# Kernel tuning notes

Hardware: AMD Instinct MI355X
Metric: run time of the kernel (lower is better)

Reference implementation:

```python
import jax, jax.numpy as jnp
import numpy as np

B = 32768
IN_DIM, OUT_DIM, VAR_DIM = 2, 3, 50
KER_DIMS = [1024, 1024, 1024, 1024]
NSTEPS = 32  # fixed-step RK4 stand-in for adaptive odeint over t in [0, 1]


def setup_inputs() -> dict:
    key = jax.random.key(0)
    ks = jax.random.split(key, 11)
    x = jax.random.normal(ks[0], (B, IN_DIM), dtype=jnp.float32)
    dims = [VAR_DIM] + KER_DIMS + [VAR_DIM]
    inp = {"x": x}
    for i, (d1, d2) in enumerate(zip(dims[:-1], dims[1:])):
        # torch Linear(d1+1, d2): weight (d2, d1+1); stored here as (d1+1, d2)
        bound = 1.0 / np.sqrt(d1 + 1)
        inp[f"W{i}"] = jax.random.uniform(ks[1 + 2 * i], (d1 + 1, d2), jnp.float32, -bound, bound)
        inp[f"b{i}"] = jax.random.uniform(ks[2 + 2 * i], (d2,), jnp.float32, -bound, bound)
    return inp


def _odefunc(t, y, Ws, bs):
    # Each layer: concat time column, Linear, ReLU (except last) -- matches ODEfunc.forward
    out = y
    n = len(Ws)
    for i in range(n):
        tcol = jnp.full((out.shape[0], 1), t, dtype=out.dtype)
        h = jnp.concatenate([out, tcol], axis=1)
        out = h @ Ws[i] + bs[i]
        if i < n - 1:
            out = jax.nn.relu(out)
    return out


def _integrate(x, Ws, bs):
    # Pad input into var_dim state: out[:, :in_dim] = x, rest zeros
    y0 = jnp.zeros((x.shape[0], VAR_DIM), dtype=x.dtype).at[:, : x.shape[1]].set(x)
    dt = jnp.asarray(1.0 / NSTEPS, dtype=x.dtype)
    ts = jnp.arange(NSTEPS, dtype=x.dtype) * dt

    def step(y, t):
        k1 = _odefunc(t, y, Ws, bs)
        k2 = _odefunc(t + dt * 0.5, y + dt * 0.5 * k1, Ws, bs)
        k3 = _odefunc(t + dt * 0.5, y + dt * 0.5 * k2, Ws, bs)
        k4 = _odefunc(t + dt, y + dt * k3, Ws, bs)
        return y + (dt / 6.0) * (k1 + 2.0 * k2 + 2.0 * k3 + k4), None

    y1, _ = jax.lax.scan(step, y0, ts)
    return y1[:, :OUT_DIM]


def reference(x, W0, b0, W1, b1, W2, b2, W3, b3, W4, b4):
    Ws = (W0, W1, W2, W3, W4)
    bs = (b0, b1, b2, b3, b4)
    return _integrate(x, Ws, bs)
```

## Files before the change

kernel.cpp:

```cpp
#include <hip/hip_runtime.h>
#include <hip/hip_bf16.h>
#include <stdint.h>


typedef __bf16 bf16_t;
typedef bf16_t bf16x8 __attribute__((ext_vector_type(8)));
typedef float  f32x4  __attribute__((ext_vector_type(4)));

#define DEVI static __device__ __forceinline__

DEVI void gload_lds16(const bf16_t* gsrc, bf16_t* ldst) {
  __builtin_amdgcn_global_load_lds(
      (const __attribute__((address_space(1))) uint32_t*)gsrc,
      (__attribute__((address_space(3))) uint32_t*)ldst,
      16, 0, 0);
}

template<int K>
__global__ __launch_bounds__(512, 2) void gemm256(
    const bf16_t* __restrict__ A,
    const bf16_t* __restrict__ BT,
    const float* __restrict__ bias,
    const float* __restrict__ wtime,
    float t,
    bf16_t* __restrict__ C, int ldc,
    int M, int N)
{
  constexpr int NT = K / 64;
  static_assert(NT >= 2, "need >=2 K-tiles");

  __shared__ __align__(16) bf16_t As[2][256][64];
  __shared__ __align__(16) bf16_t Bs[2][256][64];

  const int tid  = threadIdx.x;
  const int wave = tid >> 6;
  const int lane = tid & 63;
  const int wr = wave >> 2;
  const int wc = wave & 3;

  int wg = blockIdx.x;
  {
    const int cpx = gridDim.x >> 3;
    wg = (wg & 7) * cpx + (wg >> 3);
  }
  const int nbn = N >> 8;
  const int bm = (wg / nbn) << 8;
  const int bn = (wg % nbn) << 8;

  const int srow = lane >> 3;
  const int scol = ((lane & 7) << 3) ^ ((lane & 32) >> 1) ^ ((wave & 1) << 5);
  const bf16_t* aS = A  + (size_t)(bm + wave * 8 + srow) * K + scol;
  const bf16_t* bS = BT + (size_t)(bn + wave * 8 + srow) * K + scol;
  bf16_t* aD = &As[0][0][0] + wave * 8 * 64;
  bf16_t* bD = &Bs[0][0][0] + wave * 8 * 64;

  auto stageHalf = [&](int kt, int isB, int h) {
    const int buf = kt & 1;
    const bf16_t* src = (isB ? bS : aS) + (size_t)(h * 128) * K + kt * 64;
    bf16_t*       dst = (isB ? bD : aD) + (buf * 256 + h * 128) * 64;
    gload_lds16(src,                 dst);
    gload_lds16(src + (size_t)64 * K, dst + 64 * 64);
  };

  const int fr = lane & 15;
  const int fq = lane >> 4;
  const int rsw = ((fr & 4) << 3) ^ ((fr & 8) << 3);

  bf16x8 af[8];
  bf16x8 bfr[8];
  f32x4  acc[8][4] = {};

  auto lda_frag = [&](int buf, int mh) {
    const char* base = (const char*)&As[buf][0][0];
#pragma unroll
    for (int m = 0; m < 4; ++m)
#pragma unroll
      for (int kk = 0; kk < 2; ++kk) {
        int r  = wr * 128 + (mh * 4 + m) * 16 + fr;
        int cb = (kk * 64 + fq * 16) ^ rsw;
        af[m * 2 + kk] = *(const bf16x8*)(base + r * 128 + cb);
      }
  };
  auto ldb_frag = [&](int buf, int nh) {
    const char* base = (const char*)&Bs[buf][0][0];
#pragma unroll
    for (int n = 0; n < 2; ++n)
#pragma unroll
      for (int kk = 0; kk < 2; ++kk) {
        int r  = wc * 64 + (nh * 2 + n) * 16 + fr;
        int cb = (kk * 64 + fq * 16) ^ rsw;
        bfr[nh * 4 + n * 2 + kk] = *(const bf16x8*)(base + r * 128 + cb);
      }
  };
  auto mma_quad = [&](int mh, int nh) {
    __builtin_amdgcn_s_setprio(1);
#pragma unroll
    for (int m = 0; m < 4; ++m)
#pragma unroll
      for (int n = 0; n < 2; ++n)
#pragma unroll
        for (int kk = 0; kk < 2; ++kk)
          acc[mh * 4 + m][nh * 2 + n] = __builtin_amdgcn_mfma_f32_16x16x32_bf16(
              af[m * 2 + kk], bfr[nh * 4 + n * 2 + kk],
              acc[mh * 4 + m][nh * 2 + n], 0, 0, 0);
    __builtin_amdgcn_s_setprio(0);
  };

  stageHalf(0, 0, 0); stageHalf(0, 1, 0);
  stageHalf(0, 0, 1); stageHalf(0, 1, 1);
  stageHalf(1, 1, 0); stageHalf(1, 0, 0);
  asm volatile("s_waitcnt vmcnt(4)" ::: "memory");
  __builtin_amdgcn_s_barrier();

  for (int t2 = 0; t2 < NT; ++t2) {
    const int buf = t2 & 1;
    lda_frag(buf, 0);
    ldb_frag(buf, 0);
    if (t2 + 1 < NT) stageHalf(t2 + 1, 0, 1);
    asm volatile("s_waitcnt lgkmcnt(8)" ::: "memory");
    __builtin_amdgcn_s_barrier();
    asm volatile("s_waitcnt lgkmcnt(0)" ::: "memory");
    mma_quad(0, 0);
    __builtin_amdgcn_s_barrier();
    ldb_frag(buf, 1);
    if (t2 + 1 < NT) stageHalf(t2 + 1, 1, 1);
    __builtin_amdgcn_s_barrier();
    asm volatile("s_waitcnt lgkmcnt(0)" ::: "memory");
    mma_quad(0, 1);
    __builtin_amdgcn_s_barrier();
    lda_frag(buf, 1);
    if (t2 + 2 < NT) stageHalf(t2 + 2, 1, 0);
    __builtin_amdgcn_s_barrier();
    asm volatile("s_waitcnt lgkmcnt(0)" ::: "memory");
    mma_quad(1, 0);
    __builtin_amdgcn_s_barrier();
    if (t2 + 2 < NT) {
      stageHalf(t2 + 2, 0, 0);
      asm volatile("s_waitcnt vmcnt(4)" ::: "memory");
    } else {
      asm volatile("s_waitcnt vmcnt(0)" ::: "memory");
    }
    __builtin_amdgcn_s_barrier();
    mma_quad(1, 1);
    __builtin_amdgcn_s_barrier();
  }

#pragma unroll
  for (int n = 0; n < 4; ++n) {
    const int gcol = bn + wc * 64 + n * 16 + fr;
    const float bv = bias[gcol] + t * wtime[gcol];
#pragma unroll
    for (int m = 0; m < 8; ++m) {
      const int grow0 = bm + wr * 128 + m * 16 + (fq << 2);
#pragma unroll
      for (int r = 0; r < 4; ++r) {
        float v = acc[m][n][r] + bv;
        v = v > 0.0f ? v : 0.0f;
        C[(size_t)(grow0 + r) * ldc + gcol] = (bf16_t)v;
      }
    }
  }
}

template<int BM, int BN, int BK, int WROWS, int WCOLS, bool RELU, bool OUT_BF16>
__global__ __launch_bounds__(256) void gemm_bt(
    const bf16_t* __restrict__ A, int lda,
    const bf16_t* __restrict__ BT,
    const float* __restrict__ bias,
    const float* __restrict__ wtime,
    float t,
    void* __restrict__ Cv, int ldc,
    int M, int K)
{
  static_assert(BK == 64, "swizzle assumes BK=64");
  constexpr int MR  = BM / WROWS / 16;
  constexpr int NR  = BN / WCOLS / 16;
  constexpr int TPR = BK / 8;
  constexpr int RPW = 64 / TPR;
  constexpr int RPL = 4 * RPW;
  static_assert(BM % RPL == 0 && BN % RPL == 0, "tile staging mismatch");

  __shared__ bf16_t As[BM][BK];
  __shared__ bf16_t Bs[BN][BK];

  const int tid  = threadIdx.x;
  const int wave = tid >> 6;
  const int lane = tid & 63;
  const int wr = wave / WCOLS;
  const int wc = wave % WCOLS;
  const int bm = blockIdx.x * BM;
  const int bn = blockIdx.y * BN;
  const int lrow = lane >> 3;
  const int lcol = (((lane & 7) << 3) ^ ((lane & 32) >> 1) ^ ((wave & 1) << 5));

  const int fr = lane & 15;
  const int fq = lane >> 4;
  const int esw = ((fr & 4) << 2) ^ ((fr & 8) << 2);

  f32x4 acc[MR][NR] = {};

  for (int k0 = 0; k0 < K; k0 += BK) {
#pragma unroll
    for (int i = 0; i < BM / RPL; ++i) {
      const int rb = i * RPL + wave * RPW;
      gload_lds16(&A[(size_t)(bm + rb + lrow) * lda + k0 + lcol], &As[rb][0]);
    }
#pragma unroll
    for (int i = 0; i < BN / RPL; ++i) {
      const int rb = i * RPL + wave * RPW;
      gload_lds16(&BT[(size_t)(bn + rb + lrow) * K + k0 + lcol], &Bs[rb][0]);
    }
    __syncthreads();
#pragma unroll
    for (int kk = 0; kk < BK / 32; ++kk) {
      bf16x8 af[MR], bfr[NR];
      const int ecol = (kk * 32 + fq * 8) ^ esw;
#pragma unroll
      for (int m = 0; m < MR; ++m)
        af[m] = *(const bf16x8*)&As[wr * (BM / WROWS) + m * 16 + fr][ecol];
#pragma unroll
      for (int n = 0; n < NR; ++n)
        bfr[n] = *(const bf16x8*)&Bs[wc * (BN / WCOLS) + n * 16 + fr][ecol];
#pragma unroll
      for (int m = 0; m < MR; ++m)
#pragma unroll
        for (int n = 0; n < NR; ++n)
          acc[m][n] = __builtin_amdgcn_mfma_f32_16x16x32_bf16(
              af[m], bfr[n], acc[m][n], 0, 0, 0);
    }
    __syncthreads();
  }

#pragma unroll
  for (int n = 0; n < NR; ++n) {
    const int gcol = bn + wc * (BN / WCOLS) + n * 16 + fr;
    const float bv = bias[gcol] + t * wtime[gcol];
#pragma unroll
    for (int m = 0; m < MR; ++m) {
      const int grow0 = bm + wr * (BM / WROWS) + m * 16 + (fq << 2);
#pragma unroll
      for (int r = 0; r < 4; ++r) {
        float v = acc[m][n][r] + bv;
        if (RELU) v = v > 0.0f ? v : 0.0f;
        if constexpr (OUT_BF16)
          ((bf16_t*)Cv)[(size_t)(grow0 + r) * ldc + gcol] = (bf16_t)v;
        else
          ((float*)Cv)[(size_t)(grow0 + r) * ldc + gcol] = v;
      }
    }
  }
}

__global__ __launch_bounds__(256) void gemm_l4_rk4(
    const bf16_t* __restrict__ A, int lda,
    const bf16_t* __restrict__ BT,
    const float* __restrict__ bias,
    const float* __restrict__ wtime,
    float t,
    float* __restrict__ y, float* __restrict__ accb,
    bf16_t* __restrict__ ybf,
    float ca, float cs, int mode,
    int M, int K)
{
  constexpr int BM = 64, BN = 64, BK = 64;
  constexpr int MR = 2, NR = 2;

  __shared__ bf16_t As[BM][BK];
  __shared__ bf16_t Bs[BN][BK];

  const int tid  = threadIdx.x;
  const int wave = tid >> 6;
  const int lane = tid & 63;
  const int wr = wave >> 1;
  const int wc = wave & 1;
  const int bm = blockIdx.x * BM;
  const int lrow = lane >> 3;
  const int lcol = (((lane & 7) << 3) ^ ((lane & 32) >> 1) ^ ((wave & 1) << 5));

  const int fr = lane & 15;
  const int fq = lane >> 4;
  const int esw = ((fr & 4) << 2) ^ ((fr & 8) << 2);

  f32x4 acc[MR][NR] = {};

  for (int k0 = 0; k0 < K; k0 += BK) {
#pragma unroll
    for (int i = 0; i < 2; ++i) {
      const int rb = i * 32 + wave * 8;
      gload_lds16(&A[(size_t)(bm + rb + lrow) * lda + k0 + lcol], &As[rb][0]);
    }
#pragma unroll
    for (int i = 0; i < 2; ++i) {
      const int rb = i * 32 + wave * 8;
      gload_lds16(&BT[(size_t)(rb + lrow) * K + k0 + lcol], &Bs[rb][0]);
    }
    __syncthreads();
#pragma unroll
    for (int kk = 0; kk < 2; ++kk) {
      bf16x8 af[MR], bfr[NR];
      const int ecol = (kk * 32 + fq * 8) ^ esw;
#pragma unroll
      for (int m = 0; m < MR; ++m)
        af[m] = *(const bf16x8*)&As[wr * 32 + m * 16 + fr][ecol];
#pragma unroll
      for (int n = 0; n < NR; ++n)
        bfr[n] = *(const bf16x8*)&Bs[wc * 32 + n * 16 + fr][ecol];
#pragma unroll
      for (int m = 0; m < MR; ++m)
#pragma unroll
        for (int n = 0; n < NR; ++n)
          acc[m][n] = __builtin_amdgcn_mfma_f32_16x16x32_bf16(
              af[m], bfr[n], acc[m][n], 0, 0, 0);
    }
    __syncthreads();
  }

#pragma unroll
  for (int n = 0; n < NR; ++n) {
    const int gcol = wc * 32 + n * 16 + fr;
    const float bv = bias[gcol] + t * wtime[gcol];
#pragma unroll
    for (int m = 0; m < MR; ++m) {
      const int grow0 = bm + wr * 32 + m * 16 + (fq << 2);
#pragma unroll
      for (int r = 0; r < 4; ++r) {
        const float kv = acc[m][n][r] + bv;
        const size_t o = (size_t)(grow0 + r) * 64 + gcol;
        if (mode == 0) {
          accb[o] = kv;
          ybf[o] = (bf16_t)(y[o] + cs * kv);
        } else if (mode == 1) {
          accb[o] += ca * kv;
          ybf[o] = (bf16_t)(y[o] + cs * kv);
        } else {
          const float ny = y[o] + cs * (accb[o] + kv);
          y[o] = ny;
          ybf[o] = (bf16_t)ny;
        }
      }
    }
  }
}

__global__ void prep_weight(const float* __restrict__ W, const float* __restrict__ b,
                            bf16_t* __restrict__ WT, float* __restrict__ bias,
                            float* __restrict__ wtime,
                            int K, int N, int Kpad, int Npad)
{
  int idx = blockIdx.x * 256 + threadIdx.x;
  int total = Npad * Kpad;
  if (idx < total) {
    int n = idx / Kpad, k = idx % Kpad;
    float v = (n < N && k < K) ? W[(size_t)k * N + n] : 0.0f;
    WT[idx] = (bf16_t)v;
  }
  if (idx < Npad) {
    bias[idx]  = (idx < N) ? b[idx] : 0.0f;
    wtime[idx] = (idx < N) ? W[(size_t)K * N + idx] : 0.0f;
  }
}

__global__ void init_y(const float* __restrict__ x, float* __restrict__ y,
                       bf16_t* __restrict__ ybf, int M)
{
  int i = blockIdx.x * 256 + threadIdx.x;
  if (i < M * 64) {
    int m = i >> 6, c = i & 63;
    float v = (c < 2) ? x[m * 2 + c] : 0.0f;
    y[i] = v;
    ybf[i] = (bf16_t)v;
  }
}

__global__ void extract_out(const float* __restrict__ y, float* __restrict__ out, int M)
{
  int i = blockIdx.x * 256 + threadIdx.x;
  if (i < M * 3) {
    int m = i / 3, c = i % 3;
    out[i] = y[(size_t)m * 64 + c];
  }
}

extern "C" void kernel_launch(void* const* d_in, const int* in_sizes, int n_in,
                              void* d_out, int out_size, void* d_ws, size_t ws_size,
                              hipStream_t stream)
{
  (void)in_sizes; (void)n_in; (void)out_size; (void)ws_size;
  const int M = 32768;

  const float* x = (const float*)d_in[0];
  const float* Wp[5]; const float* bp[5];
  for (int i = 0; i < 5; ++i) {
    Wp[i] = (const float*)d_in[1 + 2 * i];
    bp[i] = (const float*)d_in[2 + 2 * i];
  }

  char* ws = (char*)d_ws; size_t off = 0;
  auto alloc = [&](size_t bytes) -> char* {
    char* p = ws + off; off += (bytes + 255) & ~(size_t)255; return p;
  };

  bf16_t* WT[5];
  WT[0] = (bf16_t*)alloc((size_t)1024 * 64 * 2);
  WT[1] = (bf16_t*)alloc((size_t)1024 * 1024 * 2);
  WT[2] = (bf16_t*)alloc((size_t)1024 * 1024 * 2);
  WT[3] = (bf16_t*)alloc((size_t)1024 * 1024 * 2);
  WT[4] = (bf16_t*)alloc((size_t)64 * 1024 * 2);
  float* bias[5]; float* wtm[5];
  for (int i = 0; i < 5; ++i) {
    int Np = (i == 4) ? 64 : 1024;
    bias[i] = (float*)alloc((size_t)Np * 4);
    wtm[i]  = (float*)alloc((size_t)Np * 4);
  }
  float*  y    = (float*)alloc((size_t)M * 64 * 4);
  float*  accb = (float*)alloc((size_t)M * 64 * 4);
  bf16_t* ybf  = (bf16_t*)alloc((size_t)M * 64 * 2);
  bf16_t* act0 = (bf16_t*)alloc((size_t)M * 1024 * 2);
  bf16_t* act1 = (bf16_t*)alloc((size_t)M * 1024 * 2);

  const int Kd[5]  = {50, 1024, 1024, 1024, 1024};
  const int Nd[5]  = {1024, 1024, 1024, 1024, 50};
  const int Kpd[5] = {64, 1024, 1024, 1024, 1024};
  const int Npd[5] = {1024, 1024, 1024, 1024, 64};
  for (int i = 0; i < 5; ++i) {
    int tot = Npd[i] * Kpd[i];
    prep_weight<<<dim3((tot + 255) / 256), 256, 0, stream>>>(
        Wp[i], bp[i], WT[i], bias[i], wtm[i], Kd[i], Nd[i], Kpd[i], Npd[i]);
  }

  init_y<<<dim3((M * 64 + 255) / 256), 256, 0, stream>>>(x, y, ybf, M);

  const float dtv = 1.0f / 32.0f;
  dim3 gL0(M / 128, 1024 / 128);
  dim3 g256(M / 256 * (1024 / 256));
  dim3 gL4(M / 64);

  auto run_net = [&](float t, float ca, float cs, int mode) {
    gemm_bt<128,128,64,2,2,true,true><<<gL0, 256, 0, stream>>>(
        ybf, 64, WT[0], bias[0], wtm[0], t, act0, 1024, M, 64);
    gemm256<1024><<<g256, 512, 0, stream>>>(
        act0, WT[1], bias[1], wtm[1], t, act1, 1024, M, 1024);
    gemm256<1024><<<g256, 512, 0, stream>>>(
        act1, WT[2], bias[2], wtm[2], t, act0, 1024, M, 1024);
    gemm256<1024><<<g256, 512, 0, stream>>>(
        act0, WT[3], bias[3], wtm[3], t, act1, 1024, M, 1024);
    gemm_l4_rk4<<<gL4, 256, 0, stream>>>(
        act1, 1024, WT[4], bias[4], wtm[4], t,
        y, accb, ybf, ca, cs, mode, M, 1024);
  };

  for (int i = 0; i < 32; ++i) {
    const float t0 = i * dtv;
    const float tm = t0 + 0.5f * dtv;
    const float t1 = t0 + dtv;
    run_net(t0, 0.0f, 0.5f * dtv, 0);
    run_net(tm, 2.0f, 0.5f * dtv, 1);
    run_net(tm, 2.0f, dtv,        1);
    run_net(t1, 0.0f, dtv / 6.0f, 2);
  }

  extract_out<<<dim3((M * 3 + 255) / 256), 256, 0, stream>>>(y, (float*)d_out, M);
}
```

Before: 39.36 ms.

## Double-buffer A fragments to prefetch next K-tile LDS reads during MFMA

Splits the A register fragments into two sets so the next K-tile's A/B fragment LDS reads are issued before the last MMA quad of the current tile, overlapping LDS latency with matrix math. It also lowers the launch bound to one block per CU, giving the compiler more registers for the extra fragments at the cost of occupancy. The pipeline now requires at least three K-tiles, and the hand-tuned waitcnt counts must match the new issue order.

```diff
diff --git a/kernel.cpp b/kernel.cpp
--- a/kernel.cpp
+++ b/kernel.cpp
@@ -17,7 +17,7 @@
 }
 
 template<int K>
-__global__ __launch_bounds__(512, 2) void gemm256(
+__global__ __launch_bounds__(512, 1) void gemm256(
     const bf16_t* __restrict__ A,
     const bf16_t* __restrict__ BT,
     const float* __restrict__ bias,
@@ -27,7 +27,7 @@
     int M, int N)
 {
   constexpr int NT = K / 64;
-  static_assert(NT >= 2, "need >=2 K-tiles");
+  static_assert(NT >= 3, "pipeline needs >=3 K-tiles");
 
   __shared__ __align__(16) bf16_t As[2][256][64];
   __shared__ __align__(16) bf16_t Bs[2][256][64];
@@ -58,7 +58,7 @@
     const int buf = kt & 1;
     const bf16_t* src = (isB ? bS : aS) + (size_t)(h * 128) * K + kt * 64;
     bf16_t*       dst = (isB ? bD : aD) + (buf * 256 + h * 128) * 64;
-    gload_lds16(src,                 dst);
+    gload_lds16(src,                  dst);
     gload_lds16(src + (size_t)64 * K, dst + 64 * 64);
   };
 
@@ -66,11 +66,11 @@
   const int fq = lane >> 4;
   const int rsw = ((fr & 4) << 3) ^ ((fr & 8) << 3);
 
-  bf16x8 af[8];
+  bf16x8 af0[8], af1[8];
   bf16x8 bfr[8];
   f32x4  acc[8][4] = {};
 
-  auto lda_frag = [&](int buf, int mh) {
+  auto lda_into = [&](bf16x8 (&dst)[8], int buf, int mh) {
     const char* base = (const char*)&As[buf][0][0];
 #pragma unroll
     for (int m = 0; m < 4; ++m)
@@ -78,10 +78,10 @@
       for (int kk = 0; kk < 2; ++kk) {
         int r  = wr * 128 + (mh * 4 + m) * 16 + fr;
         int cb = (kk * 64 + fq * 16) ^ rsw;
-        af[m * 2 + kk] = *(const bf16x8*)(base + r * 128 + cb);
+        dst[m * 2 + kk] = *(const bf16x8*)(base + r * 128 + cb);
       }
   };
-  auto ldb_frag = [&](int buf, int nh) {
+  auto ldb_half = [&](int buf, int nh) {
     const char* base = (const char*)&Bs[buf][0][0];
 #pragma unroll
     for (int n = 0; n < 2; ++n)
@@ -92,7 +92,7 @@
         bfr[nh * 4 + n * 2 + kk] = *(const bf16x8*)(base + r * 128 + cb);
       }
   };
-  auto mma_quad = [&](int mh, int nh) {
+  auto mma_quad = [&](bf16x8 (&a)[8], int mh, int nh) {
     __builtin_amdgcn_s_setprio(1);
 #pragma unroll
     for (int m = 0; m < 4; ++m)
@@ -101,7 +101,7 @@
 #pragma unroll
         for (int kk = 0; kk < 2; ++kk)
           acc[mh * 4 + m][nh * 2 + n] = __builtin_amdgcn_mfma_f32_16x16x32_bf16(
-              af[m * 2 + kk], bfr[nh * 4 + n * 2 + kk],
+              a[m * 2 + kk], bfr[nh * 4 + n * 2 + kk],
               acc[mh * 4 + m][nh * 2 + n], 0, 0, 0);
     __builtin_amdgcn_s_setprio(0);
   };
@@ -111,28 +111,27 @@
   stageHalf(1, 1, 0); stageHalf(1, 0, 0);
   asm volatile("s_waitcnt vmcnt(4)" ::: "memory");
   __builtin_amdgcn_s_barrier();
+  lda_into(af0, 0, 0);
+  ldb_half(0, 0);
 
   for (int t2 = 0; t2 < NT; ++t2) {
     const int buf = t2 & 1;
-    lda_frag(buf, 0);
-    ldb_frag(buf, 0);
+    ldb_half(buf, 1);
     if (t2 + 1 < NT) stageHalf(t2 + 1, 0, 1);
+    __builtin_amdgcn_s_barrier();
+    asm volatile("s_waitcnt lgkmcnt(4)" ::: "memory");
+    mma_quad(af0, 0, 0);
+    __builtin_amdgcn_s_barrier();
+    lda_into(af1, buf, 1);
+    if (t2 + 1 < NT) stageHalf(t2 + 1, 1, 1);
+    __builtin_amdgcn_s_barrier();
     asm volatile("s_waitcnt lgkmcnt(8)" ::: "memory");
+    mma_quad(af0, 0, 1);
+    __builtin_amdgcn_s_barrier();
+    if (t2 + 2 < NT) stageHalf(t2 + 2, 1, 0);
     __builtin_amdgcn_s_barrier();
     asm volatile("s_waitcnt lgkmcnt(0)" ::: "memory");
-    mma_quad(0, 0);
-    __builtin_amdgcn_s_barrier();
-    ldb_frag(buf, 1);
-    if (t2 + 1 < NT) stageHalf(t2 + 1, 1, 1);
-    __builtin_amdgcn_s_barrier();
-    asm volatile("s_waitcnt lgkmcnt(0)" ::: "memory");
-    mma_quad(0, 1);
-    __builtin_amdgcn_s_barrier();
-    lda_frag(buf, 1);
-    if (t2 + 2 < NT) stageHalf(t2 + 2, 1, 0);
-    __builtin_amdgcn_s_barrier();
-    asm volatile("s_waitcnt lgkmcnt(0)" ::: "memory");
-    mma_quad(1, 0);
+    mma_quad(af1, 1, 0);
     __builtin_amdgcn_s_barrier();
     if (t2 + 2 < NT) {
       stageHalf(t2 + 2, 0, 0);
@@ -141,7 +140,11 @@
       asm volatile("s_waitcnt vmcnt(0)" ::: "memory");
     }
     __builtin_amdgcn_s_barrier();
-    mma_quad(1, 1);
+    if (t2 + 1 < NT) {
+      lda_into(af0, buf ^ 1, 0);
+      ldb_half(buf ^ 1, 0);
+    }
+    mma_quad(af1, 1, 1);
     __builtin_amdgcn_s_barrier();
   }
 
```

Result: slower. 42.76 ms (+8.6%).
